# Optimization experiments

Hardware: AMD Instinct MI355X
Metric: run time of the kernel (lower is better)

## Reference

```python
import jax, jax.numpy as jnp
import numpy as np

B, T, N, F = 4, 24, 4096, 128
DIM, DIM_ATTN, RANK, HEAD = 128, 128, 32, 4
HEAD_DIM = DIM_ATTN // HEAD


def setup_inputs() -> dict:
    key = jax.random.key(0)
    ks = jax.random.split(key, 6)
    x = jax.random.normal(ks[0], (B, T, N, F), dtype=jnp.float32)
    # nn.Linear(dim, dim_attn): weight (out, in), bias (out,)
    Wq = jax.random.normal(ks[1], (DIM_ATTN, DIM), dtype=jnp.float32) / np.sqrt(DIM)
    bq = jnp.zeros((DIM_ATTN,), dtype=jnp.float32)
    # low-rank key parameter (rank, head, head_dim)
    key_param = jax.random.normal(ks[2], (RANK, HEAD, HEAD_DIM), dtype=jnp.float32)
    # nn.Linear(dim, dim)
    Wv = jax.random.normal(ks[3], (DIM, DIM), dtype=jnp.float32) / np.sqrt(DIM)
    bv = jnp.zeros((DIM,), dtype=jnp.float32)
    alpha = jnp.full((HEAD, 1), np.log(9.0), dtype=jnp.float32)
    beta = jnp.full((HEAD, 1), np.log(0.01), dtype=jnp.float32)
    return {"x": x, "Wq": Wq, "bq": bq, "key_param": key_param,
            "Wv": Wv, "bv": bv, "alpha": alpha, "beta": beta}


def reference(x, Wq, bq, key_param, Wv, bv, alpha, beta):
    b, t, n, f = x.shape
    q = (x @ Wq.T + bq).reshape(b, t, n, HEAD, HEAD_DIM)
    # scores over the rank dimension
    attn = jnp.einsum('btnhd,rhd->btnhr', q, key_param) / np.sqrt(HEAD_DIM)
    xv = (x @ Wv.T + bv).reshape(b, t, n, HEAD, HEAD_DIM)
    # stage 1: softmax over rank (last axis), aggregate values into rank slots
    v = jnp.einsum('btnhr,btnhd->btrhd', jax.nn.softmax(attn, axis=-1), xv)
    # stage 2: softmax over nodes (axis -3 == n), redistribute to nodes
    v = jnp.einsum('btnhr,btrhd->btnhd', jax.nn.softmax(attn, axis=-3), v)
    # sigmoid-gated residual mix; alpha/beta (head,1) broadcast over d
    v = jax.nn.sigmoid(alpha) * xv + jax.nn.sigmoid(beta) * v
    return v.reshape(b, t, n, f)
```

## Files before the change

kernel.cpp:

```cpp
#include <hip/hip_runtime.h>

constexpr int Nn = 4096, Fc = 128;
constexpr int Rr = 32, Hh = 4, Dd = 32;
constexpr int BT = 96;
constexpr float SCALE = 0.17677669529663687f;

constexpr size_t OFF_V1  = 0;
constexpr size_t OFF_Z   = (size_t)BT * Hh * Rr * Dd;
constexpr size_t OFF_BQK = OFF_Z + (size_t)BT * Hh * Rr;
constexpr size_t OFF_V1Z = OFF_BQK + 128;
constexpr size_t OFF_U   = OFF_V1Z + (size_t)BT * Hh * Dd * Rr / 2;

constexpr int U_WKHI = 0, U_WVHI = 16384, U_WVLO = 32768;

using short8  = __attribute__((ext_vector_type(8))) short;
using floatx4 = __attribute__((ext_vector_type(4))) float;

__device__ inline ushort f2bf(float f) {
    union { float f; unsigned u; } c{f};
    unsigned r = c.u + 0x7fffu + ((c.u >> 16) & 1u);
    return (ushort)(r >> 16);
}
__device__ inline float bf2f(ushort u) {
    union { unsigned u; float f; } c{(unsigned)u << 16};
    return c.f;
}

__global__ void kprep(const float* __restrict__ Wq, const float* __restrict__ bq,
                      const float* __restrict__ Wv, const float* __restrict__ key,
                      ushort* __restrict__ U, float* __restrict__ bqk)
{
    const int idx = blockIdx.x * 256 + threadIdx.x;
    if (idx < 16384) {
        const int hr = idx >> 7, f = idx & 127;
        const int h = hr >> 5, r = hr & 31;
        float s = 0.f;
#pragma unroll
        for (int d = 0; d < 32; d++)
            s += Wq[(h * 32 + d) * 128 + f] * key[(r * 4 + h) * 32 + d];
        U[U_WKHI + idx] = f2bf(s);
    } else if (idx < 32768) {
        const int o = idx - 16384;
        const float v = Wv[o];
        const ushort h = f2bf(v);
        U[U_WVHI + o] = h;
        U[U_WVLO + o] = f2bf(v - bf2f(h));
    } else if (idx < 32768 + 128) {
        const int hr = idx - 32768;
        const int h = hr >> 5, r = hr & 31;
        float s = 0.f;
#pragma unroll
        for (int d = 0; d < 32; d++)
            s += bq[h * 32 + d] * key[(r * 4 + h) * 32 + d];
        bqk[hr] = s;
    }
}

__global__ __launch_bounds__(256, 3)
void ka(const float* __restrict__ x, const float* __restrict__ bv,
        const ushort* __restrict__ U, const float* __restrict__ bqk,
        float* __restrict__ v1, float* __restrict__ Z)
{
    __shared__ __align__(16) char lds[54272];
    ushort* xh = (ushort*)lds;

    const int t = threadIdx.x;
    const int w = t >> 6, lane = t & 63;
    const int quad = lane >> 4, l15 = lane & 15;
    const int bt = blockIdx.y;

    char* wsc = lds + 17408 + w * 9216;
    ushort* eT  = (ushort*)wsc;
    ushort* xvT = (ushort*)(wsc + 4608);

    const ushort* WKh = U + U_WKHI;
    const ushort* Wvh = U + U_WVHI;

    float bvv[2], bqkv[2];
#pragma unroll
    for (int i = 0; i < 2; i++) {
        bvv[i]  = bv[32 * w + 16 * i + l15];
        bqkv[i] = bqk[32 * w + 16 * i + l15];
    }

    floatx4 accV1[2][2];
#pragma unroll
    for (int i = 0; i < 2; i++)
#pragma unroll
        for (int j = 0; j < 2; j++) accV1[i][j] = (floatx4)0.f;
    float zacc[2] = {0.f, 0.f};

#pragma unroll 1
    for (int it = 0; it < 4; it++) {
        const int n0 = (blockIdx.x * 4 + it) * 64;
        __syncthreads();
        const float4* xg = (const float4*)(x + ((size_t)bt * Nn + n0) * Fc);
#pragma unroll
        for (int i = 0; i < 8; i++) {
            const int idx = i * 256 + t;
            const int row = idx >> 5, c4 = idx & 31;
            float4 v = xg[idx];
            ushort4 hv;
            hv.x = f2bf(v.x); hv.y = f2bf(v.y); hv.z = f2bf(v.z); hv.w = f2bf(v.w);
            *(ushort4*)&xh[row * 136 + c4 * 4] = hv;
        }
        __syncthreads();

        floatx4 acca[4][2], accv[4][2];
#pragma unroll
        for (int mt = 0; mt < 4; mt++)
#pragma unroll
            for (int nt = 0; nt < 2; nt++) {
                acca[mt][nt] = (floatx4)0.f;
                accv[mt][nt] = (floatx4)0.f;
            }

#pragma unroll
        for (int kc = 0; kc < 4; kc++) {
            short8 ah[4];
#pragma unroll
            for (int mt = 0; mt < 4; mt++)
                ah[mt] = *(const short8*)&xh[(16 * mt + l15) * 136 + kc * 32 + quad * 8];
            short8 kb2[2], vb[2];
#pragma unroll
            for (int nt = 0; nt < 2; nt++) {
                const int off = (32 * w + 16 * nt + l15) * 128 + kc * 32 + quad * 8;
                kb2[nt] = *(const short8*)&WKh[off];
                vb[nt]  = *(const short8*)&Wvh[off];
            }
#pragma unroll
            for (int mt = 0; mt < 4; mt++)
#pragma unroll
                for (int nt = 0; nt < 2; nt++) {
                    acca[mt][nt] = __builtin_amdgcn_mfma_f32_16x16x32_bf16(ah[mt], kb2[nt], acca[mt][nt], 0, 0, 0);
                    accv[mt][nt] = __builtin_amdgcn_mfma_f32_16x16x32_bf16(ah[mt], vb[nt],  accv[mt][nt], 0, 0, 0);
                }
        }

#pragma unroll
        for (int mt = 0; mt < 4; mt++)
#pragma unroll
            for (int rt = 0; rt < 2; rt++)
#pragma unroll
                for (int reg = 0; reg < 4; reg++) {
                    const int row = 16 * mt + 4 * quad + reg;
                    const float e = __expf((acca[mt][rt][reg] + bqkv[rt]) * SCALE);
                    eT[(16 * rt + l15) * 72 + row] = f2bf(e);
                    zacc[rt] += e;
                }

        float s = 0.f;
#pragma unroll
        for (int r = 0; r < 32; r++) s += bf2f(eT[r * 72 + lane]);
        const float sinv = 1.f / s;

#pragma unroll
        for (int mt = 0; mt < 4; mt++)
#pragma unroll
            for (int reg = 0; reg < 4; reg++) {
                const int row = 16 * mt + 4 * quad + reg;
                const float sw = __shfl(sinv, row);
#pragma unroll
                for (int nt = 0; nt < 2; nt++) {
                    const float v = (accv[mt][nt][reg] + bvv[nt]) * sw;
                    xvT[(16 * nt + l15) * 72 + row] = f2bf(v);
                }
            }

#pragma unroll
        for (int kn = 0; kn < 2; kn++) {
            short8 ae[2], bx[2];
#pragma unroll
            for (int i = 0; i < 2; i++) {
                ae[i] = *(const short8*)&eT[(16 * i + l15) * 72 + kn * 32 + quad * 8];
                bx[i] = *(const short8*)&xvT[(16 * i + l15) * 72 + kn * 32 + quad * 8];
            }
#pragma unroll
            for (int mt = 0; mt < 2; mt++)
#pragma unroll
                for (int nt = 0; nt < 2; nt++)
                    accV1[mt][nt] = __builtin_amdgcn_mfma_f32_16x16x32_bf16(ae[mt], bx[nt], accV1[mt][nt], 0, 0, 0);
        }
    }

#pragma unroll
    for (int rt = 0; rt < 2; rt++) {
        float zr = zacc[rt];
        zr += __shfl_xor(zr, 16);
        zr += __shfl_xor(zr, 32);
        if (quad == 0)
            atomicAdd(&Z[((size_t)bt * Hh + w) * Rr + 16 * rt + l15], zr);
    }
    float* v1b = v1 + ((size_t)bt * Hh + w) * Rr * Dd;
#pragma unroll
    for (int mt = 0; mt < 2; mt++)
#pragma unroll
        for (int nt = 0; nt < 2; nt++)
#pragma unroll
            for (int reg = 0; reg < 4; reg++)
                atomicAdd(&v1b[(16 * mt + 4 * quad + reg) * 32 + 16 * nt + l15],
                          accV1[mt][nt][reg]);
}

__global__ void k2b(const float* __restrict__ v1, const float* __restrict__ Z,
                    ushort* __restrict__ v1z)
{
    const int idx = blockIdx.x * 256 + threadIdx.x;
    const int d = idx & 31, r = (idx >> 5) & 31, hr = idx >> 10;
    const float z = Z[hr * 32 + r];
    v1z[((size_t)hr * 32 + d) * 32 + r] = f2bf(v1[idx] / z);
}

__global__ __launch_bounds__(256, 2)
void kb(const float* __restrict__ x, const float* __restrict__ bv,
        const ushort* __restrict__ U, const float* __restrict__ bqk,
        const ushort* __restrict__ v1z, const float* __restrict__ alpha,
        const float* __restrict__ beta, float* __restrict__ out)
{
    __shared__ __align__(16) char lds[67584];
    ushort* xhi = (ushort*)lds;
    ushort* xlo = (ushort*)(lds + 17408);

    const int t = threadIdx.x;
    const int w = t >> 6, lane = t & 63;
    const int quad = lane >> 4, l15 = lane & 15;
    const int bt = blockIdx.y;
    const int n0 = blockIdx.x * 64;

    char* wsc = lds + 34816 + w * 8192;
    ushort* eS = (ushort*)wsc;
    float*  fS = (float*)wsc;

    const float4* xg = (const float4*)(x + ((size_t)bt * Nn + n0) * Fc);
#pragma unroll
    for (int i = 0; i < 8; i++) {
        const int idx = i * 256 + t;
        const int row = idx >> 5, c4 = idx & 31;
        float4 v = xg[idx];
        ushort h0 = f2bf(v.x), h1 = f2bf(v.y), h2 = f2bf(v.z), h3 = f2bf(v.w);
        ushort4 hv; hv.x = h0; hv.y = h1; hv.z = h2; hv.w = h3;
        ushort4 lv; lv.x = f2bf(v.x - bf2f(h0)); lv.y = f2bf(v.y - bf2f(h1));
        lv.z = f2bf(v.z - bf2f(h2)); lv.w = f2bf(v.w - bf2f(h3));
        *(ushort4*)&xhi[row * 136 + c4 * 4] = hv;
        *(ushort4*)&xlo[row * 136 + c4 * 4] = lv;
    }
    __syncthreads();

    const ushort* WKh = U + U_WKHI;
    const ushort* Wvh = U + U_WVHI;
    const ushort* Wvl = U + U_WVLO;

    float bqkv[2], bvv[2];
#pragma unroll
    for (int i = 0; i < 2; i++) {
        bqkv[i] = bqk[32 * w + 16 * i + l15];
        bvv[i]  = bv[32 * w + 16 * i + l15];
    }

    floatx4 acca[4][2], accv[4][2];
#pragma unroll
    for (int mt = 0; mt < 4; mt++)
#pragma unroll
        for (int nt = 0; nt < 2; nt++) {
            acca[mt][nt] = (floatx4)0.f;
            accv[mt][nt] = (floatx4)0.f;
        }

#pragma unroll
    for (int kc = 0; kc < 4; kc++) {
        short8 ahi[4], alo[4];
#pragma unroll
        for (int mt = 0; mt < 4; mt++) {
            const int ro = (16 * mt + l15) * 136 + kc * 32 + quad * 8;
            ahi[mt] = *(const short8*)&xhi[ro];
            alo[mt] = *(const short8*)&xlo[ro];
        }
        short8 kb2[2], vbh[2], vbl[2];
#pragma unroll
        for (int nt = 0; nt < 2; nt++) {
            const int off = (32 * w + 16 * nt + l15) * 128 + kc * 32 + quad * 8;
            kb2[nt] = *(const short8*)&WKh[off];
            vbh[nt] = *(const short8*)&Wvh[off];
            vbl[nt] = *(const short8*)&Wvl[off];
        }
#pragma unroll
        for (int mt = 0; mt < 4; mt++)
#pragma unroll
            for (int nt = 0; nt < 2; nt++) {
                acca[mt][nt] = __builtin_amdgcn_mfma_f32_16x16x32_bf16(ahi[mt], kb2[nt], acca[mt][nt], 0, 0, 0);
                accv[mt][nt] = __builtin_amdgcn_mfma_f32_16x16x32_bf16(ahi[mt], vbh[nt], accv[mt][nt], 0, 0, 0);
                accv[mt][nt] = __builtin_amdgcn_mfma_f32_16x16x32_bf16(ahi[mt], vbl[nt], accv[mt][nt], 0, 0, 0);
                accv[mt][nt] = __builtin_amdgcn_mfma_f32_16x16x32_bf16(alo[mt], vbh[nt], accv[mt][nt], 0, 0, 0);
            }
    }

#pragma unroll
    for (int mt = 0; mt < 4; mt++)
#pragma unroll
        for (int rt = 0; rt < 2; rt++)
#pragma unroll
            for (int reg = 0; reg < 4; reg++) {
                const int row = 16 * mt + 4 * quad + reg;
                const int col = 16 * rt + l15;
                eS[row * 40 + col] =
                    f2bf(__expf((acca[mt][rt][reg] + bqkv[rt]) * SCALE));
            }

    short8 pa[4];
#pragma unroll
    for (int mt = 0; mt < 4; mt++)
        pa[mt] = *(const short8*)&eS[(16 * mt + l15) * 40 + quad * 8];
    short8 vbz[2];
#pragma unroll
    for (int dt = 0; dt < 2; dt++)
        vbz[dt] = *(const short8*)&v1z[(((size_t)bt * Hh + w) * Dd + 16 * dt + l15) * Rr + quad * 8];
    floatx4 acc2[4][2];
#pragma unroll
    for (int mt = 0; mt < 4; mt++)
#pragma unroll
        for (int dt = 0; dt < 2; dt++) {
            acc2[mt][dt] = (floatx4)0.f;
            acc2[mt][dt] = __builtin_amdgcn_mfma_f32_16x16x32_bf16(pa[mt], vbz[dt], acc2[mt][dt], 0, 0, 0);
        }

    const float sa = 1.f / (1.f + __expf(-alpha[w]));
    const float sb = 1.f / (1.f + __expf(-beta[w]));

#pragma unroll
    for (int mt = 0; mt < 4; mt++)
#pragma unroll
        for (int nt = 0; nt < 2; nt++)
#pragma unroll
            for (int reg = 0; reg < 4; reg++) {
                const int row = 16 * mt + 4 * quad + reg;
                const int col = 16 * nt + l15;
                fS[row * 32 + col] =
                    sa * (accv[mt][nt][reg] + bvv[nt]) + sb * acc2[mt][nt][reg];
            }
#pragma unroll
    for (int i = 0; i < 8; i++) {
        const int idx = i * 64 + lane;
        const int n = idx >> 3, c4 = idx & 7;
        *(float4*)&out[((size_t)bt * Nn + n0 + n) * 128 + w * 32 + c4 * 4] =
            *(const float4*)&fS[n * 32 + c4 * 4];
    }
}

extern "C" void kernel_launch(void* const* d_in, const int* in_sizes, int n_in,
                              void* d_out, int out_size, void* d_ws, size_t ws_size,
                              hipStream_t stream)
{
    const float* x     = (const float*)d_in[0];
    const float* Wq    = (const float*)d_in[1];
    const float* bq    = (const float*)d_in[2];
    const float* key   = (const float*)d_in[3];
    const float* Wv    = (const float*)d_in[4];
    const float* bv    = (const float*)d_in[5];
    const float* alpha = (const float*)d_in[6];
    const float* beta  = (const float*)d_in[7];
    float* out = (float*)d_out;

    float*  ws   = (float*)d_ws;
    float*  v1   = ws + OFF_V1;
    float*  Z    = ws + OFF_Z;
    float*  bqkp = ws + OFF_BQK;
    ushort* v1z  = (ushort*)(ws + OFF_V1Z);
    ushort* U    = (ushort*)(ws + OFF_U);

    hipMemsetAsync(v1, 0,
                   (size_t)(BT * Hh * Rr * Dd + BT * Hh * Rr) * sizeof(float),
                   stream);
    kprep<<<dim3(129), 256, 0, stream>>>(Wq, bq, Wv, key, U, bqkp);
    ka<<<dim3(16, BT), 256, 0, stream>>>(x, bv, U, bqkp, v1, Z);
    k2b<<<dim3(BT * Hh * Rr * Dd / 256), 256, 0, stream>>>(v1, Z, v1z);
    kb<<<dim3(Nn / 64, BT), 256, 0, stream>>>(x, bv, U, bqkp, v1z, alpha, beta, out);
}
```

Baseline: 553.8 us.

## Prefetch next x tile into registers and loop kb over four tiles

Both main kernels now prefetch the next 64-row x tile into registers while the current tile is computed. ka double-buffers its bf16 LDS staging and drops the leading barrier. It also replaces the LDS re-read row-sum with a shuffle-xor reduction of the softmax denominators. kb now processes four tiles per block with a grid of 16 instead of 64 column-blocks, hoisting the v1z and gate loads. This costs more registers, fewer waves per CU (ka launch bounds drop to 2), and fewer blocks in kb.

```diff
diff --git a/kernel.cpp b/kernel.cpp
--- a/kernel.cpp
+++ b/kernel.cpp
@@ -56,20 +56,20 @@
     }
 }
 
-__global__ __launch_bounds__(256, 3)
+__global__ __launch_bounds__(256, 2)
 void ka(const float* __restrict__ x, const float* __restrict__ bv,
         const ushort* __restrict__ U, const float* __restrict__ bqk,
         float* __restrict__ v1, float* __restrict__ Z)
 {
-    __shared__ __align__(16) char lds[54272];
-    ushort* xh = (ushort*)lds;
+    __shared__ __align__(16) char lds[71680];
 
     const int t = threadIdx.x;
     const int w = t >> 6, lane = t & 63;
     const int quad = lane >> 4, l15 = lane & 15;
     const int bt = blockIdx.y;
-
-    char* wsc = lds + 17408 + w * 9216;
+    constexpr int NT = 4;
+
+    char* wsc = lds + 34816 + w * 9216;
     ushort* eT  = (ushort*)wsc;
     ushort* xvT = (ushort*)(wsc + 4608);
 
@@ -90,16 +90,20 @@
         for (int j = 0; j < 2; j++) accV1[i][j] = (floatx4)0.f;
     float zacc[2] = {0.f, 0.f};
 
+    const float* xbase = x + ((size_t)bt * Nn + blockIdx.x * (NT * 64)) * Fc;
+
+    float4 xr[8];
+#pragma unroll
+    for (int i = 0; i < 8; i++) xr[i] = ((const float4*)xbase)[i * 256 + t];
+
 #pragma unroll 1
-    for (int it = 0; it < 4; it++) {
-        const int n0 = (blockIdx.x * 4 + it) * 64;
-        __syncthreads();
-        const float4* xg = (const float4*)(x + ((size_t)bt * Nn + n0) * Fc);
+    for (int it = 0; it < NT; ++it) {
+        ushort* xh = (ushort*)(lds + (it & 1) * 17408);
 #pragma unroll
         for (int i = 0; i < 8; i++) {
             const int idx = i * 256 + t;
             const int row = idx >> 5, c4 = idx & 31;
-            float4 v = xg[idx];
+            float4 v = xr[i];
             ushort4 hv;
             hv.x = f2bf(v.x); hv.y = f2bf(v.y); hv.z = f2bf(v.z); hv.w = f2bf(v.w);
             *(ushort4*)&xh[row * 136 + c4 * 4] = hv;
@@ -137,34 +141,43 @@
                 }
         }
 
-#pragma unroll
-        for (int mt = 0; mt < 4; mt++)
-#pragma unroll
-            for (int rt = 0; rt < 2; rt++)
-#pragma unroll
-                for (int reg = 0; reg < 4; reg++) {
-                    const int row = 16 * mt + 4 * quad + reg;
-                    const float e = __expf((acca[mt][rt][reg] + bqkv[rt]) * SCALE);
-                    eT[(16 * rt + l15) * 72 + row] = f2bf(e);
-                    zacc[rt] += e;
-                }
-
-        float s = 0.f;
-#pragma unroll
-        for (int r = 0; r < 32; r++) s += bf2f(eT[r * 72 + lane]);
-        const float sinv = 1.f / s;
-
+        if (it + 1 < NT) {
+            const float4* xg = (const float4*)(xbase + (size_t)(it + 1) * 64 * Fc);
+#pragma unroll
+            for (int i = 0; i < 8; i++) xr[i] = xg[i * 256 + t];
+        }
+
+        float sloc[4][4];
 #pragma unroll
         for (int mt = 0; mt < 4; mt++)
 #pragma unroll
             for (int reg = 0; reg < 4; reg++) {
-                const int row = 16 * mt + 4 * quad + reg;
-                const float sw = __shfl(sinv, row);
-#pragma unroll
-                for (int nt = 0; nt < 2; nt++) {
-                    const float v = (accv[mt][nt][reg] + bvv[nt]) * sw;
-                    xvT[(16 * nt + l15) * 72 + row] = f2bf(v);
-                }
+                const int n = 16 * mt + 4 * quad + reg;
+                const float e0 = __expf((acca[mt][0][reg] + bqkv[0]) * SCALE);
+                const float e1 = __expf((acca[mt][1][reg] + bqkv[1]) * SCALE);
+                eT[l15 * 72 + n]        = f2bf(e0);
+                eT[(16 + l15) * 72 + n] = f2bf(e1);
+                zacc[0] += e0; zacc[1] += e1;
+                sloc[mt][reg] = e0 + e1;
+            }
+#pragma unroll
+        for (int m = 1; m < 16; m <<= 1)
+#pragma unroll
+            for (int mt = 0; mt < 4; mt++)
+#pragma unroll
+                for (int reg = 0; reg < 4; reg++)
+                    sloc[mt][reg] += __shfl_xor(sloc[mt][reg], m);
+
+#pragma unroll
+        for (int mt = 0; mt < 4; mt++)
+#pragma unroll
+            for (int reg = 0; reg < 4; reg++) {
+                const int n = 16 * mt + 4 * quad + reg;
+                const float sw = 1.f / sloc[mt][reg];
+#pragma unroll
+                for (int nt = 0; nt < 2; nt++)
+                    xvT[(16 * nt + l15) * 72 + n] =
+                        f2bf((accv[mt][nt][reg] + bvv[nt]) * sw);
             }
 
 #pragma unroll
@@ -225,27 +238,12 @@
     const int w = t >> 6, lane = t & 63;
     const int quad = lane >> 4, l15 = lane & 15;
     const int bt = blockIdx.y;
-    const int n0 = blockIdx.x * 64;
+    constexpr int NT = 4;
 
     char* wsc = lds + 34816 + w * 8192;
     ushort* eS = (ushort*)wsc;
     float*  fS = (float*)wsc;
 
-    const float4* xg = (const float4*)(x + ((size_t)bt * Nn + n0) * Fc);
-#pragma unroll
-    for (int i = 0; i < 8; i++) {
-        const int idx = i * 256 + t;
-        const int row = idx >> 5, c4 = idx & 31;
-        float4 v = xg[idx];
-        ushort h0 = f2bf(v.x), h1 = f2bf(v.y), h2 = f2bf(v.z), h3 = f2bf(v.w);
-        ushort4 hv; hv.x = h0; hv.y = h1; hv.z = h2; hv.w = h3;
-        ushort4 lv; lv.x = f2bf(v.x - bf2f(h0)); lv.y = f2bf(v.y - bf2f(h1));
-        lv.z = f2bf(v.z - bf2f(h2)); lv.w = f2bf(v.w - bf2f(h3));
-        *(ushort4*)&xhi[row * 136 + c4 * 4] = hv;
-        *(ushort4*)&xlo[row * 136 + c4 * 4] = lv;
-    }
-    __syncthreads();
-
     const ushort* WKh = U + U_WKHI;
     const ushort* Wvh = U + U_WVHI;
     const ushort* Wvl = U + U_WVLO;
@@ -256,93 +254,124 @@
         bqkv[i] = bqk[32 * w + 16 * i + l15];
         bvv[i]  = bv[32 * w + 16 * i + l15];
     }
-
-    floatx4 acca[4][2], accv[4][2];
-#pragma unroll
-    for (int mt = 0; mt < 4; mt++)
-#pragma unroll
-        for (int nt = 0; nt < 2; nt++) {
-            acca[mt][nt] = (floatx4)0.f;
-            accv[mt][nt] = (floatx4)0.f;
-        }
-
-#pragma unroll
-    for (int kc = 0; kc < 4; kc++) {
-        short8 ahi[4], alo[4];
-#pragma unroll
-        for (int mt = 0; mt < 4; mt++) {
-            const int ro = (16 * mt + l15) * 136 + kc * 32 + quad * 8;
-            ahi[mt] = *(const short8*)&xhi[ro];
-            alo[mt] = *(const short8*)&xlo[ro];
-        }
-        short8 kb2[2], vbh[2], vbl[2];
-#pragma unroll
-        for (int nt = 0; nt < 2; nt++) {
-            const int off = (32 * w + 16 * nt + l15) * 128 + kc * 32 + quad * 8;
-            kb2[nt] = *(const short8*)&WKh[off];
-            vbh[nt] = *(const short8*)&Wvh[off];
-            vbl[nt] = *(const short8*)&Wvl[off];
-        }
-#pragma unroll
-        for (int mt = 0; mt < 4; mt++)
-#pragma unroll
-            for (int nt = 0; nt < 2; nt++) {
-                acca[mt][nt] = __builtin_amdgcn_mfma_f32_16x16x32_bf16(ahi[mt], kb2[nt], acca[mt][nt], 0, 0, 0);
-                accv[mt][nt] = __builtin_amdgcn_mfma_f32_16x16x32_bf16(ahi[mt], vbh[nt], accv[mt][nt], 0, 0, 0);
-                accv[mt][nt] = __builtin_amdgcn_mfma_f32_16x16x32_bf16(ahi[mt], vbl[nt], accv[mt][nt], 0, 0, 0);
-                accv[mt][nt] = __builtin_amdgcn_mfma_f32_16x16x32_bf16(alo[mt], vbh[nt], accv[mt][nt], 0, 0, 0);
-            }
-    }
-
-#pragma unroll
-    for (int mt = 0; mt < 4; mt++)
-#pragma unroll
-        for (int rt = 0; rt < 2; rt++)
-#pragma unroll
-            for (int reg = 0; reg < 4; reg++) {
-                const int row = 16 * mt + 4 * quad + reg;
-                const int col = 16 * rt + l15;
-                eS[row * 40 + col] =
-                    f2bf(__expf((acca[mt][rt][reg] + bqkv[rt]) * SCALE));
-            }
-
-    short8 pa[4];
-#pragma unroll
-    for (int mt = 0; mt < 4; mt++)
-        pa[mt] = *(const short8*)&eS[(16 * mt + l15) * 40 + quad * 8];
     short8 vbz[2];
 #pragma unroll
     for (int dt = 0; dt < 2; dt++)
         vbz[dt] = *(const short8*)&v1z[(((size_t)bt * Hh + w) * Dd + 16 * dt + l15) * Rr + quad * 8];
-    floatx4 acc2[4][2];
-#pragma unroll
-    for (int mt = 0; mt < 4; mt++)
-#pragma unroll
-        for (int dt = 0; dt < 2; dt++) {
-            acc2[mt][dt] = (floatx4)0.f;
-            acc2[mt][dt] = __builtin_amdgcn_mfma_f32_16x16x32_bf16(pa[mt], vbz[dt], acc2[mt][dt], 0, 0, 0);
-        }
-
     const float sa = 1.f / (1.f + __expf(-alpha[w]));
     const float sb = 1.f / (1.f + __expf(-beta[w]));
 
-#pragma unroll
-    for (int mt = 0; mt < 4; mt++)
-#pragma unroll
-        for (int nt = 0; nt < 2; nt++)
-#pragma unroll
-            for (int reg = 0; reg < 4; reg++) {
-                const int row = 16 * mt + 4 * quad + reg;
-                const int col = 16 * nt + l15;
-                fS[row * 32 + col] =
-                    sa * (accv[mt][nt][reg] + bvv[nt]) + sb * acc2[mt][nt][reg];
-            }
-#pragma unroll
-    for (int i = 0; i < 8; i++) {
-        const int idx = i * 64 + lane;
-        const int n = idx >> 3, c4 = idx & 7;
-        *(float4*)&out[((size_t)bt * Nn + n0 + n) * 128 + w * 32 + c4 * 4] =
-            *(const float4*)&fS[n * 32 + c4 * 4];
+    const float* xbase = x + ((size_t)bt * Nn + blockIdx.x * (NT * 64)) * Fc;
+    float* obase = out + ((size_t)bt * Nn + blockIdx.x * (NT * 64)) * Fc;
+
+    float4 xr[8];
+#pragma unroll
+    for (int i = 0; i < 8; i++) xr[i] = ((const float4*)xbase)[i * 256 + t];
+
+#pragma unroll 1
+    for (int it = 0; it < NT; ++it) {
+#pragma unroll
+        for (int i = 0; i < 8; i++) {
+            const int idx = i * 256 + t;
+            const int row = idx >> 5, c4 = idx & 31;
+            float4 v = xr[i];
+            ushort h0 = f2bf(v.x), h1 = f2bf(v.y), h2 = f2bf(v.z), h3 = f2bf(v.w);
+            ushort4 hv; hv.x = h0; hv.y = h1; hv.z = h2; hv.w = h3;
+            ushort4 lv; lv.x = f2bf(v.x - bf2f(h0)); lv.y = f2bf(v.y - bf2f(h1));
+            lv.z = f2bf(v.z - bf2f(h2)); lv.w = f2bf(v.w - bf2f(h3));
+            *(ushort4*)&xhi[row * 136 + c4 * 4] = hv;
+            *(ushort4*)&xlo[row * 136 + c4 * 4] = lv;
+        }
+        __syncthreads();
+
+        floatx4 acca[4][2], accv[4][2];
+#pragma unroll
+        for (int mt = 0; mt < 4; mt++)
+#pragma unroll
+            for (int nt = 0; nt < 2; nt++) {
+                acca[mt][nt] = (floatx4)0.f;
+                accv[mt][nt] = (floatx4)0.f;
+            }
+
+#pragma unroll
+        for (int kc = 0; kc < 4; kc++) {
+            short8 ahi[4], alo[4];
+#pragma unroll
+            for (int mt = 0; mt < 4; mt++) {
+                const int ro = (16 * mt + l15) * 136 + kc * 32 + quad * 8;
+                ahi[mt] = *(const short8*)&xhi[ro];
+                alo[mt] = *(const short8*)&xlo[ro];
+            }
+            short8 kb2[2], vbh[2], vbl[2];
+#pragma unroll
+            for (int nt = 0; nt < 2; nt++) {
+                const int off = (32 * w + 16 * nt + l15) * 128 + kc * 32 + quad * 8;
+                kb2[nt] = *(const short8*)&WKh[off];
+                vbh[nt] = *(const short8*)&Wvh[off];
+                vbl[nt] = *(const short8*)&Wvl[off];
+            }
+#pragma unroll
+            for (int mt = 0; mt < 4; mt++)
+#pragma unroll
+                for (int nt = 0; nt < 2; nt++) {
+                    acca[mt][nt] = __builtin_amdgcn_mfma_f32_16x16x32_bf16(ahi[mt], kb2[nt], acca[mt][nt], 0, 0, 0);
+                    accv[mt][nt] = __builtin_amdgcn_mfma_f32_16x16x32_bf16(ahi[mt], vbh[nt], accv[mt][nt], 0, 0, 0);
+                    accv[mt][nt] = __builtin_amdgcn_mfma_f32_16x16x32_bf16(ahi[mt], vbl[nt], accv[mt][nt], 0, 0, 0);
+                    accv[mt][nt] = __builtin_amdgcn_mfma_f32_16x16x32_bf16(alo[mt], vbh[nt], accv[mt][nt], 0, 0, 0);
+                }
+        }
+
+        if (it + 1 < NT) {
+            const float4* xg = (const float4*)(xbase + (size_t)(it + 1) * 64 * Fc);
+#pragma unroll
+            for (int i = 0; i < 8; i++) xr[i] = xg[i * 256 + t];
+        }
+
+#pragma unroll
+        for (int mt = 0; mt < 4; mt++)
+#pragma unroll
+            for (int rt = 0; rt < 2; rt++)
+#pragma unroll
+                for (int reg = 0; reg < 4; reg++) {
+                    const int row = 16 * mt + 4 * quad + reg;
+                    const int col = 16 * rt + l15;
+                    eS[row * 40 + col] =
+                        f2bf(__expf((acca[mt][rt][reg] + bqkv[rt]) * SCALE));
+                }
+
+        short8 pa[4];
+#pragma unroll
+        for (int mt = 0; mt < 4; mt++)
+            pa[mt] = *(const short8*)&eS[(16 * mt + l15) * 40 + quad * 8];
+        floatx4 acc2[4][2];
+#pragma unroll
+        for (int mt = 0; mt < 4; mt++)
+#pragma unroll
+            for (int dt = 0; dt < 2; dt++) {
+                acc2[mt][dt] = (floatx4)0.f;
+                acc2[mt][dt] = __builtin_amdgcn_mfma_f32_16x16x32_bf16(pa[mt], vbz[dt], acc2[mt][dt], 0, 0, 0);
+            }
+
+#pragma unroll
+        for (int mt = 0; mt < 4; mt++)
+#pragma unroll
+            for (int nt = 0; nt < 2; nt++)
+#pragma unroll
+                for (int reg = 0; reg < 4; reg++) {
+                    const int row = 16 * mt + 4 * quad + reg;
+                    const int col = 16 * nt + l15;
+                    fS[row * 32 + col] =
+                        sa * (accv[mt][nt][reg] + bvv[nt]) + sb * acc2[mt][nt][reg];
+                }
+        float* op = obase + (size_t)it * 64 * Fc;
+#pragma unroll
+        for (int i = 0; i < 8; i++) {
+            const int idx = i * 64 + lane;
+            const int n = idx >> 3, c4 = idx & 7;
+            *(float4*)&op[(size_t)n * 128 + w * 32 + c4 * 4] =
+                *(const float4*)&fS[n * 32 + c4 * 4];
+        }
+        __syncthreads();
     }
 }
 
@@ -373,5 +402,5 @@
     kprep<<<dim3(129), 256, 0, stream>>>(Wq, bq, Wv, key, U, bqkp);
     ka<<<dim3(16, BT), 256, 0, stream>>>(x, bv, U, bqkp, v1, Z);
     k2b<<<dim3(BT * Hh * Rr * Dd / 256), 256, 0, stream>>>(v1, Z, v1z);
-    kb<<<dim3(Nn / 64, BT), 256, 0, stream>>>(x, bv, U, bqkp, v1z, alpha, beta, out);
-}
+    kb<<<dim3(16, BT), 256, 0, stream>>>(x, bv, U, bqkp, v1z, alpha, beta, out);
+}
```

New measurement: 522.6 us. 1.06x faster.
